# Optimization experiments

Measured on AMD Instinct MI355X. Metric: run time of the kernel, lower is better.

The kernel has to match this reference:

```python
import jax, jax.numpy as jnp
import numpy as np

EPS = 1e-5

def _bn(x, g, b):
    # BatchNorm1d in training mode: stats over (batch, length) dims, biased var
    mean = jnp.mean(x, axis=(0, 2), keepdims=True)
    var = jnp.var(x, axis=(0, 2), keepdims=True)
    return (x - mean) * jax.lax.rsqrt(var + EPS) * g[None, :, None] + b[None, :, None]

def _conv1x1(x, w, b):
    # pointwise Conv1d: [B,C,T] x [O,C] -> [B,O,T]
    return jnp.einsum('bct,oc->bot', x, w) + b[None, :, None]

def setup_inputs() -> dict:
    key = jax.random.key(0)
    ks = jax.random.split(key, 4)
    B, C, T = 32, 1024, 2048
    x = jax.random.normal(ks[0], (B, C, T), dtype=jnp.float32)
    w1 = jax.random.normal(ks[1], (256, 1024), dtype=jnp.float32) * (1.0 / np.sqrt(1024))
    w2 = jax.random.normal(ks[2], (64, 256), dtype=jnp.float32) * (1.0 / np.sqrt(256))
    return {
        'x': x,
        'bn1_g': jnp.ones((1024,), jnp.float32), 'bn1_b': jnp.zeros((1024,), jnp.float32),
        'w1': w1, 'b1': jnp.zeros((256,), jnp.float32),
        'bn2_g': jnp.ones((256,), jnp.float32), 'bn2_b': jnp.zeros((256,), jnp.float32),
        'w2': w2, 'b2': jnp.zeros((64,), jnp.float32),
    }

def reference(x, bn1_g, bn1_b, w1, b1, bn2_g, bn2_b, w2, b2):
    # reduction layer: BN -> 1x1 conv -> ReLU (1024 -> 256)
    h = jax.nn.relu(_conv1x1(_bn(x, bn1_g, bn1_b), w1, b1))
    # out layer: BN -> 1x1 conv, no activation (256 -> 64)
    out = _conv1x1(_bn(h, bn2_g, bn2_b), w2, b2)
    o = out.shape[1]
    mu = out[:, : o // 2, :]
    logvar = out[:, o // 2 :, :]
    return (mu, logvar)
```

## Files before the change

kernel.cpp:

```cpp
#include <hip/hip_runtime.h>

#define B_  32
#define C1  1024
#define C2  256
#define T_  2048
#define EPSF 1e-5f
#define CPAD 72

typedef __attribute__((ext_vector_type(8))) short bf16x8;
typedef __attribute__((ext_vector_type(4))) float f32x4;

static __device__ __forceinline__ unsigned short f2bf(float f) {
    union { float f; unsigned u; } v; v.f = f;
    unsigned r = v.u + 0x7fffu + ((v.u >> 16) & 1u);
    return (unsigned short)(r >> 16);
}
static __device__ __forceinline__ void g2l16(const void* g, void* l) {
    __builtin_amdgcn_global_load_lds(
        (const __attribute__((address_space(1))) unsigned int*)g,
        (__attribute__((address_space(3))) unsigned int*)l, 16, 0, 0);
}

__global__ __launch_bounds__(256) void k_prep(const float* __restrict__ x,
        unsigned short* __restrict__ xT, float* __restrict__ psum, float* __restrict__ psq) {
    __shared__ unsigned short tile[64 * CPAD];
    __shared__ float red[256];
    int ct = blockIdx.x, b = blockIdx.y, tid = threadIdx.x;
    int c0 = ct * 64;
    int cl = tid >> 2, t4 = tid & 3;
    const float* xrow = x + (size_t)b * C1 * T_ + (size_t)(c0 + cl) * T_;
    float s = 0.f, sq = 0.f;
    for (int t0 = 0; t0 < T_; t0 += 64) {
        #pragma unroll
        for (int j = 0; j < 4; ++j) {
            int tl = j * 16 + t4 * 4;
            float4 v = *(const float4*)(xrow + t0 + tl);
            s  += v.x + v.y + v.z + v.w;
            sq += v.x * v.x + v.y * v.y + v.z * v.z + v.w * v.w;
            tile[(tl + 0) * CPAD + cl] = f2bf(v.x);
            tile[(tl + 1) * CPAD + cl] = f2bf(v.y);
            tile[(tl + 2) * CPAD + cl] = f2bf(v.z);
            tile[(tl + 3) * CPAD + cl] = f2bf(v.w);
        }
        __syncthreads();
        #pragma unroll
        for (int j = 0; j < 2; ++j) {
            int w = tid + j * 256;
            int tl = w >> 3, cu = w & 7;
            uint4 vv = *(const uint4*)&tile[tl * CPAD + cu * 8];
            *(uint4*)&xT[((size_t)b * T_ + t0 + tl) * C1 + c0 + cu * 8] = vv;
        }
        __syncthreads();
    }
    red[tid] = s; __syncthreads();
    if (tid < 64)
        psum[(size_t)b * C1 + c0 + tid] = red[4*tid] + red[4*tid+1] + red[4*tid+2] + red[4*tid+3];
    __syncthreads();
    red[tid] = sq; __syncthreads();
    if (tid < 64)
        psq[(size_t)b * C1 + c0 + tid]  = red[4*tid] + red[4*tid+1] + red[4*tid+2] + red[4*tid+3];
}

__global__ __launch_bounds__(256) void k_bnstat1(const float* __restrict__ psum,
        const float* __restrict__ psq, const float* __restrict__ g1,
        const float* __restrict__ bb1, float* __restrict__ sc1, float* __restrict__ sh1) {
    int c = blockIdx.x * 256 + threadIdx.x;
    float s = 0.f, q = 0.f;
    for (int b = 0; b < B_; ++b) {
        s += psum[(size_t)b * C1 + c];
        q += psq[(size_t)b * C1 + c];
    }
    const float n = (float)(B_ * T_);
    float m = s / n;
    float sc = g1[c] * rsqrtf(q / n - m * m + EPSF);
    sc1[c] = sc;
    sh1[c] = bb1[c] - m * sc;
}

__global__ __launch_bounds__(256) void k_fold1(const float* __restrict__ w1,
        const float* __restrict__ b1, const float* __restrict__ sc1,
        const float* __restrict__ sh1, unsigned short* __restrict__ w1e,
        float* __restrict__ b1e) {
    int o = blockIdx.x, tid = threadIdx.x;
    int c = tid * 4;
    float4 w  = ((const float4*)(w1 + (size_t)o * C1))[tid];
    float4 sc = *(const float4*)(sc1 + c);
    float4 sh = *(const float4*)(sh1 + c);
    float p = w.x * sh.x + w.y * sh.y + w.z * sh.z + w.w * sh.w;
    uint2 pk;
    pk.x = (unsigned)f2bf(w.x * sc.x) | ((unsigned)f2bf(w.y * sc.y) << 16);
    pk.y = (unsigned)f2bf(w.z * sc.z) | ((unsigned)f2bf(w.w * sc.w) << 16);
    *((uint2*)(w1e + (size_t)o * C1 + c)) = pk;
    int wave = tid >> 6, lane = tid & 63;
    for (int m = 1; m < 64; m <<= 1) p += __shfl_xor(p, m);
    __shared__ float rs[4];
    if (lane == 0) rs[wave] = p;
    __syncthreads();
    if (tid == 0) b1e[o] = b1[o] + rs[0] + rs[1] + rs[2] + rs[3];
}

__global__ __launch_bounds__(256, 2) void k_gemm1(const unsigned short* __restrict__ xT,
        const unsigned short* __restrict__ w1e, const float* __restrict__ b1e,
        unsigned short* __restrict__ hT, float* __restrict__ p2s, float* __restrict__ p2q) {
    __shared__ unsigned short sA[2][256 * 32];
    __shared__ unsigned short sB[2][128 * 32];
    int bn = blockIdx.x, b = blockIdx.y;
    int tid = threadIdx.x;
    int wave = tid >> 6, lane = tid & 63;
    int wm = wave >> 1, wn = wave & 1;
    int l15 = lane & 15, q = lane >> 4;
    f32x4 acc[8][4] = {};
    const unsigned short* xblk = xT + ((size_t)b * T_ + (size_t)bn * 128) * C1;

    auto stage = [&](int buf, int k0) {
        #pragma unroll
        for (int i = 0; i < 4; ++i) {
            int idx = (wave * 4 + i) * 64 + lane;
            int row = idx >> 2, cq = idx & 3;
            g2l16(w1e + (size_t)row * C1 + k0 + cq * 8, &sA[buf][(wave * 4 + i) * 512]);
        }
        #pragma unroll
        for (int i = 0; i < 2; ++i) {
            int idx = (wave * 2 + i) * 64 + lane;
            int row = idx >> 2, cq = idx & 3;
            g2l16(xblk + (size_t)row * C1 + k0 + cq * 8, &sB[buf][(wave * 2 + i) * 512]);
        }
    };

    stage(0, 0);
    __syncthreads();
    int cur = 0;
    for (int kt = 0; kt < 32; ++kt) {
        if (kt < 31) stage(cur ^ 1, (kt + 1) * 32);
        bf16x8 bfr[4];
        #pragma unroll
        for (int ni = 0; ni < 4; ++ni)
            bfr[ni] = *((const bf16x8*)&sB[cur][(wn * 64 + ni * 16 + l15) * 32 + q * 8]);
        #pragma unroll
        for (int mi = 0; mi < 8; ++mi) {
            bf16x8 af = *((const bf16x8*)&sA[cur][(wm * 128 + mi * 16 + l15) * 32 + q * 8]);
            #pragma unroll
            for (int ni = 0; ni < 4; ++ni)
                acc[mi][ni] = __builtin_amdgcn_mfma_f32_16x16x32_bf16(af, bfr[ni], acc[mi][ni], 0, 0, 0);
        }
        __syncthreads();
        cur ^= 1;
    }
    int obase = wm * 128;
    int tbase = bn * 128 + wn * 64;
    int prow = (b * 16 + bn) * 2 + wn;
    #pragma unroll
    for (int mi = 0; mi < 8; ++mi) {
        int og = obase + mi * 16 + q * 4;
        float4 bias = *(const float4*)&b1e[og];
        float s0 = 0, s1 = 0, s2 = 0, s3 = 0, q0 = 0, q1 = 0, q2 = 0, q3 = 0;
        #pragma unroll
        for (int ni = 0; ni < 4; ++ni) {
            int t = tbase + ni * 16 + l15;
            float v0 = fmaxf(acc[mi][ni][0] + bias.x, 0.f);
            float v1 = fmaxf(acc[mi][ni][1] + bias.y, 0.f);
            float v2 = fmaxf(acc[mi][ni][2] + bias.z, 0.f);
            float v3 = fmaxf(acc[mi][ni][3] + bias.w, 0.f);
            s0 += v0; q0 += v0 * v0;  s1 += v1; q1 += v1 * v1;
            s2 += v2; q2 += v2 * v2;  s3 += v3; q3 += v3 * v3;
            uint2 pk;
            pk.x = (unsigned)f2bf(v0) | ((unsigned)f2bf(v1) << 16);
            pk.y = (unsigned)f2bf(v2) | ((unsigned)f2bf(v3) << 16);
            *(uint2*)&hT[((size_t)b * T_ + t) * C2 + og] = pk;
        }
        #pragma unroll
        for (int m = 1; m <= 8; m <<= 1) {
            s0 += __shfl_xor(s0, m); s1 += __shfl_xor(s1, m);
            s2 += __shfl_xor(s2, m); s3 += __shfl_xor(s3, m);
            q0 += __shfl_xor(q0, m); q1 += __shfl_xor(q1, m);
            q2 += __shfl_xor(q2, m); q3 += __shfl_xor(q3, m);
        }
        if (l15 == 0) {
            p2s[(size_t)(og + 0) * 1024 + prow] = s0;
            p2s[(size_t)(og + 1) * 1024 + prow] = s1;
            p2s[(size_t)(og + 2) * 1024 + prow] = s2;
            p2s[(size_t)(og + 3) * 1024 + prow] = s3;
            p2q[(size_t)(og + 0) * 1024 + prow] = q0;
            p2q[(size_t)(og + 1) * 1024 + prow] = q1;
            p2q[(size_t)(og + 2) * 1024 + prow] = q2;
            p2q[(size_t)(og + 3) * 1024 + prow] = q3;
        }
    }
}

__global__ __launch_bounds__(256) void k_bnstat2(const float* __restrict__ p2s,
        const float* __restrict__ p2q, const float* __restrict__ g2,
        const float* __restrict__ bb2, float* __restrict__ sc2, float* __restrict__ sh2) {
    int c = blockIdx.x, tid = threadIdx.x;
    float4 a  = *(const float4*)(p2s + (size_t)c * 1024 + tid * 4);
    float4 qv = *(const float4*)(p2q + (size_t)c * 1024 + tid * 4);
    float s = a.x + a.y + a.z + a.w;
    float q = qv.x + qv.y + qv.z + qv.w;
    for (int m = 1; m < 64; m <<= 1) { s += __shfl_xor(s, m); q += __shfl_xor(q, m); }
    __shared__ float rs[4], rq[4];
    int wave = tid >> 6, lane = tid & 63;
    if (lane == 0) { rs[wave] = s; rq[wave] = q; }
    __syncthreads();
    if (tid == 0) {
        s = rs[0] + rs[1] + rs[2] + rs[3];
        q = rq[0] + rq[1] + rq[2] + rq[3];
        const float n = (float)(B_ * T_);
        float m0 = s / n;
        float sc = g2[c] * rsqrtf(q / n - m0 * m0 + EPSF);
        sc2[c] = sc;
        sh2[c] = bb2[c] - m0 * sc;
    }
}

__global__ __launch_bounds__(256) void k_fold2(const float* __restrict__ w2,
        const float* __restrict__ b2, const float* __restrict__ sc2,
        const float* __restrict__ sh2, unsigned short* __restrict__ w2e,
        float* __restrict__ b2e) {
    int o = blockIdx.x, tid = threadIdx.x;
    float w = w2[(size_t)o * C2 + tid];
    w2e[(size_t)o * C2 + tid] = f2bf(w * sc2[tid]);
    float p = w * sh2[tid];
    int wave = tid >> 6, lane = tid & 63;
    for (int m = 1; m < 64; m <<= 1) p += __shfl_xor(p, m);
    __shared__ float rs[4];
    if (lane == 0) rs[wave] = p;
    __syncthreads();
    if (tid == 0) b2e[o] = b2[o] + rs[0] + rs[1] + rs[2] + rs[3];
}

__global__ __launch_bounds__(256) void k_gemm2(const unsigned short* __restrict__ hT,
        const unsigned short* __restrict__ w2e, const float* __restrict__ b2e,
        float* __restrict__ out) {
    __shared__ unsigned short sA[64 * 32];
    __shared__ unsigned short sB[128 * 32];
    int bn = blockIdx.x, b = blockIdx.y;
    int tid = threadIdx.x;
    int wave = tid >> 6, lane = tid & 63;
    int l15 = lane & 15, q = lane >> 4;
    f32x4 acc[4][2] = {};
    const unsigned short* hblk = hT + ((size_t)b * T_ + (size_t)bn * 128) * C2;

    for (int k0 = 0; k0 < C2; k0 += 32) {
        {
            int idx = wave * 64 + lane;
            int row = idx >> 2, cq = idx & 3;
            g2l16(w2e + (size_t)row * C2 + k0 + cq * 8, &sA[wave * 512]);
        }
        #pragma unroll
        for (int i = 0; i < 2; ++i) {
            int idx = (wave * 2 + i) * 64 + lane;
            int row = idx >> 2, cq = idx & 3;
            g2l16(hblk + (size_t)row * C2 + k0 + cq * 8, &sB[(wave * 2 + i) * 512]);
        }
        __syncthreads();
        bf16x8 af[4], bfr[2];
        #pragma unroll
        for (int mi = 0; mi < 4; ++mi)
            af[mi] = *((const bf16x8*)&sA[(mi * 16 + l15) * 32 + q * 8]);
        #pragma unroll
        for (int ni = 0; ni < 2; ++ni)
            bfr[ni] = *((const bf16x8*)&sB[(wave * 32 + ni * 16 + l15) * 32 + q * 8]);
        #pragma unroll
        for (int mi = 0; mi < 4; ++mi)
            #pragma unroll
            for (int ni = 0; ni < 2; ++ni)
                acc[mi][ni] = __builtin_amdgcn_mfma_f32_16x16x32_bf16(af[mi], bfr[ni], acc[mi][ni], 0, 0, 0);
        __syncthreads();
    }
    int tbase = bn * 128 + wave * 32;
    #pragma unroll
    for (int mi = 0; mi < 4; ++mi) {
        #pragma unroll
        for (int reg = 0; reg < 4; ++reg) {
            int o = mi * 16 + q * 4 + reg;
            float bias = b2e[o];
            size_t base = (o < 32)
                ? ((size_t)b * 32 * T_ + (size_t)o * T_)
                : (2097152u + (size_t)b * 32 * T_ + (size_t)(o - 32) * T_);
            #pragma unroll
            for (int ni = 0; ni < 2; ++ni) {
                int t = tbase + ni * 16 + l15;
                out[base + t] = acc[mi][ni][reg] + bias;
            }
        }
    }
}

extern "C" void kernel_launch(void* const* d_in, const int* in_sizes, int n_in,
                              void* d_out, int out_size, void* d_ws, size_t ws_size,
                              hipStream_t stream) {
    const float* x   = (const float*)d_in[0];
    const float* g1  = (const float*)d_in[1];
    const float* bb1 = (const float*)d_in[2];
    const float* w1  = (const float*)d_in[3];
    const float* b1  = (const float*)d_in[4];
    const float* g2  = (const float*)d_in[5];
    const float* bb2 = (const float*)d_in[6];
    const float* w2  = (const float*)d_in[7];
    const float* b2  = (const float*)d_in[8];
    float* out = (float*)d_out;

    char* ws = (char*)d_ws;
    float* b1e  = (float*)(ws + 0);
    float* b2e  = (float*)(ws + 4096);
    float* psum = (float*)(ws + 8192);
    float* psq  = (float*)(ws + 139264);
    float* p2s  = (float*)(ws + 270336);
    float* p2q  = (float*)(ws + 1318912);
    unsigned short* w1e = (unsigned short*)(ws + 2367488);
    unsigned short* w2e = (unsigned short*)(ws + 2891776);
    float* sc1 = (float*)(ws + 2924544);
    float* sh1 = (float*)(ws + 2928640);
    float* sc2 = (float*)(ws + 2932736);
    float* sh2 = (float*)(ws + 2933760);
    unsigned short* xT  = (unsigned short*)(ws + 2934784);
    unsigned short* hT  = (unsigned short*)(ws + 2934784 + 134217728);

    k_prep   <<<dim3(16, 32), dim3(256), 0, stream>>>(x, xT, psum, psq);
    k_bnstat1<<<dim3(4),      dim3(256), 0, stream>>>(psum, psq, g1, bb1, sc1, sh1);
    k_fold1  <<<dim3(256),    dim3(256), 0, stream>>>(w1, b1, sc1, sh1, w1e, b1e);
    k_gemm1  <<<dim3(16, 32), dim3(256), 0, stream>>>(xT, w1e, b1e, hT, p2s, p2q);
    k_bnstat2<<<dim3(256),    dim3(256), 0, stream>>>(p2s, p2q, g2, bb2, sc2, sh2);
    k_fold2  <<<dim3(64),     dim3(256), 0, stream>>>(w2, b2, sc2, sh2, w2e, b2e);
    k_gemm2  <<<dim3(16, 32), dim3(256), 0, stream>>>(hT, w2e, b2e, out);
}
```

Baseline: 507.1 us.

## Fuse x transpose and bf16 conversion into GEMM1 operand loading

The prep kernel now only computes per-channel sums and sums of squares, and no longer writes a transposed bf16 copy of x (128 MB). GEMM1 reads fp32 x directly, converts it to bf16 in registers and writes it transposed into padded LDS. The register prefetch overlaps with the MFMA loop. This removes a large write-then-read round trip through HBM. In exchange GEMM1 reads twice as many bytes for its B operand (fp32 instead of bf16), does 2-byte scattered LDS stores, and carries extra register pressure.

```diff
diff --git a/kernel.cpp b/kernel.cpp
--- a/kernel.cpp
+++ b/kernel.cpp
@@ -5,7 +5,7 @@
 #define C2  256
 #define T_  2048
 #define EPSF 1e-5f
-#define CPAD 72
+#define BPITCH 40
 
 typedef __attribute__((ext_vector_type(8))) short bf16x8;
 typedef __attribute__((ext_vector_type(4))) float f32x4;
@@ -21,44 +21,25 @@
         (__attribute__((address_space(3))) unsigned int*)l, 16, 0, 0);
 }
 
-__global__ __launch_bounds__(256) void k_prep(const float* __restrict__ x,
-        unsigned short* __restrict__ xT, float* __restrict__ psum, float* __restrict__ psq) {
-    __shared__ unsigned short tile[64 * CPAD];
-    __shared__ float red[256];
+__global__ __launch_bounds__(256) void k_stats(const float* __restrict__ x,
+        float* __restrict__ psum, float* __restrict__ psq) {
     int ct = blockIdx.x, b = blockIdx.y, tid = threadIdx.x;
     int c0 = ct * 64;
     int cl = tid >> 2, t4 = tid & 3;
-    const float* xrow = x + (size_t)b * C1 * T_ + (size_t)(c0 + cl) * T_;
+    const float* xrow = x + (size_t)b * C1 * T_ + (size_t)(c0 + cl) * T_ + t4 * 4;
     float s = 0.f, sq = 0.f;
-    for (int t0 = 0; t0 < T_; t0 += 64) {
-        #pragma unroll
-        for (int j = 0; j < 4; ++j) {
-            int tl = j * 16 + t4 * 4;
-            float4 v = *(const float4*)(xrow + t0 + tl);
-            s  += v.x + v.y + v.z + v.w;
-            sq += v.x * v.x + v.y * v.y + v.z * v.z + v.w * v.w;
-            tile[(tl + 0) * CPAD + cl] = f2bf(v.x);
-            tile[(tl + 1) * CPAD + cl] = f2bf(v.y);
-            tile[(tl + 2) * CPAD + cl] = f2bf(v.z);
-            tile[(tl + 3) * CPAD + cl] = f2bf(v.w);
-        }
-        __syncthreads();
-        #pragma unroll
-        for (int j = 0; j < 2; ++j) {
-            int w = tid + j * 256;
-            int tl = w >> 3, cu = w & 7;
-            uint4 vv = *(const uint4*)&tile[tl * CPAD + cu * 8];
-            *(uint4*)&xT[((size_t)b * T_ + t0 + tl) * C1 + c0 + cu * 8] = vv;
-        }
-        __syncthreads();
-    }
-    red[tid] = s; __syncthreads();
-    if (tid < 64)
-        psum[(size_t)b * C1 + c0 + tid] = red[4*tid] + red[4*tid+1] + red[4*tid+2] + red[4*tid+3];
-    __syncthreads();
-    red[tid] = sq; __syncthreads();
-    if (tid < 64)
-        psq[(size_t)b * C1 + c0 + tid]  = red[4*tid] + red[4*tid+1] + red[4*tid+2] + red[4*tid+3];
+    #pragma unroll 4
+    for (int t0 = 0; t0 < T_; t0 += 16) {
+        float4 v = *(const float4*)(xrow + t0);
+        s  += v.x + v.y + v.z + v.w;
+        sq += v.x * v.x + v.y * v.y + v.z * v.z + v.w * v.w;
+    }
+    s  += __shfl_xor(s, 1);  s  += __shfl_xor(s, 2);
+    sq += __shfl_xor(sq, 1); sq += __shfl_xor(sq, 2);
+    if (t4 == 0) {
+        psum[(size_t)b * C1 + c0 + cl] = s;
+        psq [(size_t)b * C1 + c0 + cl] = sq;
+    }
 }
 
 __global__ __launch_bounds__(256) void k_bnstat1(const float* __restrict__ psum,
@@ -99,43 +80,62 @@
     if (tid == 0) b1e[o] = b1[o] + rs[0] + rs[1] + rs[2] + rs[3];
 }
 
-__global__ __launch_bounds__(256, 2) void k_gemm1(const unsigned short* __restrict__ xT,
+__global__ __launch_bounds__(256, 2) void k_gemm1(const float* __restrict__ x,
         const unsigned short* __restrict__ w1e, const float* __restrict__ b1e,
         unsigned short* __restrict__ hT, float* __restrict__ p2s, float* __restrict__ p2q) {
-    __shared__ unsigned short sA[2][256 * 32];
-    __shared__ unsigned short sB[2][128 * 32];
+    __shared__ alignas(16) unsigned short sA[2][256 * 32];
+    __shared__ alignas(16) unsigned short sB[2][128 * BPITCH];
     int bn = blockIdx.x, b = blockIdx.y;
     int tid = threadIdx.x;
     int wave = tid >> 6, lane = tid & 63;
     int wm = wave >> 1, wn = wave & 1;
     int l15 = lane & 15, q = lane >> 4;
     f32x4 acc[8][4] = {};
-    const unsigned short* xblk = xT + ((size_t)b * T_ + (size_t)bn * 128) * C1;
-
-    auto stage = [&](int buf, int k0) {
+
+    int kk = tid >> 3, tc = tid & 7;
+    const float* xbase = x + (size_t)b * C1 * T_ + (size_t)kk * T_ + (size_t)bn * 128 + tc * 4;
+
+    auto stageA = [&](int buf, int k0) {
         #pragma unroll
         for (int i = 0; i < 4; ++i) {
             int idx = (wave * 4 + i) * 64 + lane;
             int row = idx >> 2, cq = idx & 3;
             g2l16(w1e + (size_t)row * C1 + k0 + cq * 8, &sA[buf][(wave * 4 + i) * 512]);
         }
-        #pragma unroll
-        for (int i = 0; i < 2; ++i) {
-            int idx = (wave * 2 + i) * 64 + lane;
-            int row = idx >> 2, cq = idx & 3;
-            g2l16(xblk + (size_t)row * C1 + k0 + cq * 8, &sB[buf][(wave * 2 + i) * 512]);
-        }
     };
-
-    stage(0, 0);
+    float4 rB[4];
+    auto loadB = [&](int k0) {
+        #pragma unroll
+        for (int j = 0; j < 4; ++j)
+            rB[j] = *(const float4*)(xbase + (size_t)k0 * T_ + j * 32);
+    };
+    auto writeB = [&](int buf) {
+        #pragma unroll
+        for (int j = 0; j < 4; ++j) {
+            int t = tc * 4 + j * 32;
+            unsigned short* p = &sB[buf][t * BPITCH + kk];
+            p[0 * BPITCH] = f2bf(rB[j].x);
+            p[1 * BPITCH] = f2bf(rB[j].y);
+            p[2 * BPITCH] = f2bf(rB[j].z);
+            p[3 * BPITCH] = f2bf(rB[j].w);
+        }
+    };
+
+    loadB(0);
+    stageA(0, 0);
+    writeB(0);
     __syncthreads();
     int cur = 0;
     for (int kt = 0; kt < 32; ++kt) {
-        if (kt < 31) stage(cur ^ 1, (kt + 1) * 32);
+        int nxt = cur ^ 1;
+        if (kt < 31) {
+            loadB((kt + 1) * 32);
+            stageA(nxt, (kt + 1) * 32);
+        }
         bf16x8 bfr[4];
         #pragma unroll
         for (int ni = 0; ni < 4; ++ni)
-            bfr[ni] = *((const bf16x8*)&sB[cur][(wn * 64 + ni * 16 + l15) * 32 + q * 8]);
+            bfr[ni] = *((const bf16x8*)&sB[cur][(wn * 64 + ni * 16 + l15) * BPITCH + q * 8]);
         #pragma unroll
         for (int mi = 0; mi < 8; ++mi) {
             bf16x8 af = *((const bf16x8*)&sA[cur][(wm * 128 + mi * 16 + l15) * 32 + q * 8]);
@@ -143,8 +143,9 @@
             for (int ni = 0; ni < 4; ++ni)
                 acc[mi][ni] = __builtin_amdgcn_mfma_f32_16x16x32_bf16(af, bfr[ni], acc[mi][ni], 0, 0, 0);
         }
+        if (kt < 31) writeB(nxt);
         __syncthreads();
-        cur ^= 1;
+        cur = nxt;
     }
     int obase = wm * 128;
     int tbase = bn * 128 + wn * 64;
@@ -231,8 +232,8 @@
 __global__ __launch_bounds__(256) void k_gemm2(const unsigned short* __restrict__ hT,
         const unsigned short* __restrict__ w2e, const float* __restrict__ b2e,
         float* __restrict__ out) {
-    __shared__ unsigned short sA[64 * 32];
-    __shared__ unsigned short sB[128 * 32];
+    __shared__ alignas(16) unsigned short sA[64 * 32];
+    __shared__ alignas(16) unsigned short sB[128 * 32];
     int bn = blockIdx.x, b = blockIdx.y;
     int tid = threadIdx.x;
     int wave = tid >> 6, lane = tid & 63;
@@ -313,13 +314,12 @@
     float* sh1 = (float*)(ws + 2928640);
     float* sc2 = (float*)(ws + 2932736);
     float* sh2 = (float*)(ws + 2933760);
-    unsigned short* xT  = (unsigned short*)(ws + 2934784);
-    unsigned short* hT  = (unsigned short*)(ws + 2934784 + 134217728);
-
-    k_prep   <<<dim3(16, 32), dim3(256), 0, stream>>>(x, xT, psum, psq);
+    unsigned short* hT  = (unsigned short*)(ws + 2934784);
+
+    k_stats  <<<dim3(16, 32), dim3(256), 0, stream>>>(x, psum, psq);
     k_bnstat1<<<dim3(4),      dim3(256), 0, stream>>>(psum, psq, g1, bb1, sc1, sh1);
     k_fold1  <<<dim3(256),    dim3(256), 0, stream>>>(w1, b1, sc1, sh1, w1e, b1e);
-    k_gemm1  <<<dim3(16, 32), dim3(256), 0, stream>>>(xT, w1e, b1e, hT, p2s, p2q);
+    k_gemm1  <<<dim3(16, 32), dim3(256), 0, stream>>>(x, w1e, b1e, hT, p2s, p2q);
     k_bnstat2<<<dim3(256),    dim3(256), 0, stream>>>(p2s, p2q, g2, bb2, sc2, sh2);
     k_fold2  <<<dim3(64),     dim3(256), 0, stream>>>(w2, b2, sc2, sh2, w2e, b2e);
     k_gemm2  <<<dim3(16, 32), dim3(256), 0, stream>>>(hT, w2e, b2e, out);
```

Result: faster. 485.1 us (-4.3%).
